# Performance work log

Hardware: AMD Instinct MI355X
Metric: run time of the kernel (lower is better)

Reference implementation:

```python
import jax, jax.numpy as jnp
import numpy as np

N = 8192
E = 524288
IN_DIM = 128
HID = 256
OUT_DIM = 128
N_LAYERS = 3
N_HEADS = 4
HEAD_DIM = HID // N_HEADS


def setup_inputs() -> dict:
    key = jax.random.key(0)
    ks = jax.random.split(key, 12)
    s = 0.05
    return {
        "x": jax.random.normal(ks[0], (N, IN_DIM), dtype=jnp.float32),
        "edge_index": jax.random.randint(ks[1], (2, E), 0, N, dtype=jnp.int64),
        "W_in": jax.random.normal(ks[2], (HID, IN_DIM), dtype=jnp.float32) * s,
        "b_in": jnp.zeros((HID,), dtype=jnp.float32),
        "plasticity": jnp.ones((N_LAYERS,), dtype=jnp.float32),
        "synaptic": jnp.ones((N_LAYERS,), dtype=jnp.float32),
        "in_proj_w": jax.random.normal(ks[3], (3 * HID, HID), dtype=jnp.float32) * s,
        "in_proj_b": jnp.zeros((3 * HID,), dtype=jnp.float32),
        "out_proj_w": jax.random.normal(ks[4], (HID, HID), dtype=jnp.float32) * s,
        "out_proj_b": jnp.zeros((HID,), dtype=jnp.float32),
        "W_out": jax.random.normal(ks[5], (OUT_DIM, HID), dtype=jnp.float32) * s,
        "b_out": jnp.zeros((OUT_DIM,), dtype=jnp.float32),
    }


def _forward(x, edge_index, W_in, b_in, plasticity, synaptic,
             in_proj_w, in_proj_b, out_proj_w, out_proj_b, W_out, b_out):
    src, dst = edge_index[0], edge_index[1]  # x_j = x[src], aggregate at dst (source_to_target)
    x = x @ W_in.T + b_in  # [N, HID]
    for i in range(N_LAYERS):
        x = x * jax.nn.sigmoid(plasticity[i])
        # message: x_j * sigmoid(synaptic) (scalar edge weight); aggr='add'
        agg = jax.ops.segment_sum(x[src], dst, num_segments=N)  # gather-scatter-add
        x = jax.nn.leaky_relu(agg * jax.nn.sigmoid(synaptic[i]), negative_slope=0.01)
    # MultiheadAttention over all N nodes (seq_len=N, batch=1)
    qkv = x @ in_proj_w.T + in_proj_b  # [N, 3*HID]
    q, k, v = jnp.split(qkv, 3, axis=-1)
    q = q.reshape(N, N_HEADS, HEAD_DIM).transpose(1, 0, 2)  # [h, n, d]
    k = k.reshape(N, N_HEADS, HEAD_DIM).transpose(1, 0, 2)
    v = v.reshape(N, N_HEADS, HEAD_DIM).transpose(1, 0, 2)
    scores = jnp.einsum("hnd,hmd->hnm", q, k) / np.sqrt(HEAD_DIM).astype(np.float32)
    attn = jax.nn.softmax(scores, axis=-1)
    o = jnp.einsum("hnm,hmd->hnd", attn, v)  # [h, n, d]
    o = o.transpose(1, 0, 2).reshape(N, HID)
    x = o @ out_proj_w.T + out_proj_b
    return x @ W_out.T + b_out  # [N, OUT_DIM]


def reference(x, edge_index, W_in, b_in, plasticity, synaptic,
              in_proj_w, in_proj_b, out_proj_w, out_proj_b, W_out, b_out):
    return _forward(x, edge_index, W_in, b_in, plasticity, synaptic,
                    in_proj_w, in_proj_b, out_proj_w, out_proj_b, W_out, b_out)
```

## Files before the change

kernel.cpp:

```cpp
#include <hip/hip_runtime.h>
#include <hip/hip_bf16.h>
#include <float.h>

#define N_NODES 8192
#define NEDGE   524288
#define IND     128
#define HID     256
#define OUTD    128
#define NHEAD   4
#define HD      64

typedef short short8 __attribute__((ext_vector_type(8)));
typedef float f32x4 __attribute__((ext_vector_type(4)));

__device__ __forceinline__ float sigmoidf_(float x) { return 1.0f / (1.0f + expf(-x)); }

__device__ __forceinline__ unsigned short f2bf(float f) {
    __hip_bfloat16 b = __float2bfloat16(f);
    return __builtin_bit_cast(unsigned short, b);
}
__device__ __forceinline__ float bf2f(unsigned short u) {
    __hip_bfloat16 b = __builtin_bit_cast(__hip_bfloat16, u);
    return __bfloat162float(b);
}
__device__ __forceinline__ void split3(float x, unsigned short& a, unsigned short& b, unsigned short& c) {
    a = f2bf(x); float r = x - bf2f(a);
    b = f2bf(r); r = r - bf2f(b);
    c = f2bf(r);
}
__device__ __forceinline__ unsigned int pack2(float lo, float hi) {
    return (unsigned int)f2bf(lo) | ((unsigned int)f2bf(hi) << 16);
}

__device__ __forceinline__ void gll16(const void* g, void* l) {
    __builtin_amdgcn_global_load_lds(
        (const __attribute__((address_space(1))) void*)g,
        (__attribute__((address_space(3))) void*)l, 16, 0, 0);
}

__global__ __launch_bounds__(256) void gemm_bias_kernel(
    const float* __restrict__ A, const float* __restrict__ W,
    const float* __restrict__ bias, float* __restrict__ C,
    int M, int Nn, int K)
{
    __shared__ float As[64][33];
    __shared__ float Ws[64][33];
    const int t  = threadIdx.x;
    const int tx = t & 15, ty = t >> 4;
    const int m0 = blockIdx.x * 64, n0 = blockIdx.y * 64;
    const int lr = t >> 2;
    const int lc = (t & 3) * 8;

    float acc[4][4] = {};
    for (int kk = 0; kk < K; kk += 32) {
        const float* Ap = A + (size_t)(m0 + lr) * K + kk + lc;
        const float* Wp = W + (size_t)(n0 + lr) * K + kk + lc;
        float4 a0 = *(const float4*)(Ap);
        float4 a1 = *(const float4*)(Ap + 4);
        float4 w0 = *(const float4*)(Wp);
        float4 w1 = *(const float4*)(Wp + 4);
        __syncthreads();
        As[lr][lc + 0] = a0.x; As[lr][lc + 1] = a0.y; As[lr][lc + 2] = a0.z; As[lr][lc + 3] = a0.w;
        As[lr][lc + 4] = a1.x; As[lr][lc + 5] = a1.y; As[lr][lc + 6] = a1.z; As[lr][lc + 7] = a1.w;
        Ws[lr][lc + 0] = w0.x; Ws[lr][lc + 1] = w0.y; Ws[lr][lc + 2] = w0.z; Ws[lr][lc + 3] = w0.w;
        Ws[lr][lc + 4] = w1.x; Ws[lr][lc + 5] = w1.y; Ws[lr][lc + 6] = w1.z; Ws[lr][lc + 7] = w1.w;
        __syncthreads();
        #pragma unroll 8
        for (int k = 0; k < 32; ++k) {
            float a[4], w[4];
            #pragma unroll
            for (int i = 0; i < 4; ++i) a[i] = As[ty * 4 + i][k];
            #pragma unroll
            for (int j = 0; j < 4; ++j) w[j] = Ws[tx * 4 + j][k];
            #pragma unroll
            for (int i = 0; i < 4; ++i)
                #pragma unroll
                for (int j = 0; j < 4; ++j)
                    acc[i][j] += a[i] * w[j];
        }
    }
    #pragma unroll
    for (int i = 0; i < 4; ++i) {
        const int m = m0 + ty * 4 + i;
        #pragma unroll
        for (int j = 0; j < 4; ++j) {
            const int n = n0 + tx * 4 + j;
            C[(size_t)m * Nn + n] = acc[i][j] + bias[n];
        }
    }
}

__global__ void hist_kernel(const int* __restrict__ ei, int* __restrict__ deg)
{
    int e = blockIdx.x * blockDim.x + threadIdx.x;
    if (e < NEDGE) atomicAdd(&deg[ei[NEDGE + e]], 1);
}

__global__ __launch_bounds__(1024) void scan_kernel(
    const int* __restrict__ deg, int* __restrict__ row_ptr, int* __restrict__ cursor)
{
    __shared__ int sh[1024];
    const int t = threadIdx.x;
    int v[8]; int s = 0;
    #pragma unroll
    for (int i = 0; i < 8; ++i) { v[i] = deg[t * 8 + i]; s += v[i]; }
    sh[t] = s; __syncthreads();
    for (int off = 1; off < 1024; off <<= 1) {
        int add = (t >= off) ? sh[t - off] : 0;
        __syncthreads();
        sh[t] += add;
        __syncthreads();
    }
    int base = sh[t] - s;
    #pragma unroll
    for (int i = 0; i < 8; ++i) {
        row_ptr[t * 8 + i] = base;
        cursor[t * 8 + i]  = base;
        base += v[i];
    }
    if (t == 1023) row_ptr[N_NODES] = base;
}

__global__ void scatter_kernel(const int* __restrict__ ei, int* __restrict__ cursor,
                               int* __restrict__ esrc)
{
    int e = blockIdx.x * blockDim.x + threadIdx.x;
    if (e < NEDGE) {
        int d = ei[NEDGE + e];
        int p = atomicAdd(&cursor[d], 1);
        esrc[p] = ei[e];
    }
}

__global__ __launch_bounds__(256) void aggregate_kernel(
    const float* __restrict__ hin, float* __restrict__ hout,
    const int* __restrict__ row_ptr, const int* __restrict__ esrc,
    const float* __restrict__ plas, const float* __restrict__ syn, int layer)
{
    const int b = blockIdx.x;
    const int c = threadIdx.x;
    const int st = row_ptr[b], en = row_ptr[b + 1];
    float a0 = 0.f, a1 = 0.f, a2 = 0.f, a3 = 0.f;
    int e = st;
    for (; e + 4 <= en; e += 4) {
        int s0 = esrc[e], s1 = esrc[e + 1], s2 = esrc[e + 2], s3 = esrc[e + 3];
        a0 += hin[(size_t)s0 * HID + c];
        a1 += hin[(size_t)s1 * HID + c];
        a2 += hin[(size_t)s2 * HID + c];
        a3 += hin[(size_t)s3 * HID + c];
    }
    float acc = (a0 + a1) + (a2 + a3);
    for (; e < en; ++e) acc += hin[(size_t)esrc[e] * HID + c];
    const float scale = sigmoidf_(plas[layer]) * sigmoidf_(syn[layer]);
    float x = acc * scale;
    hout[(size_t)b * HID + c] = (x > 0.f) ? x : 0.01f * x;
}

__global__ __launch_bounds__(256) void split_kernel(
    const float* __restrict__ qkv,
    unsigned short* __restrict__ Kc0, unsigned short* __restrict__ Kc1,
    unsigned short* __restrict__ Kc2, unsigned short* __restrict__ Vt0)
{
    __shared__ unsigned short vts[64 * 80];
    const int h  = blockIdx.y;
    const int n0 = blockIdx.x * 64;
    const int t  = threadIdx.x;
    const int r  = t >> 2;
    const int n  = n0 + r;
    const int dc = (t & 3) * 16;

    {
        const float* kp = qkv + (size_t)n * 768 + 256 + h * 64 + dc;
        float kv[16];
        #pragma unroll
        for (int i = 0; i < 16; i += 4) {
            float4 f = *(const float4*)(kp + i);
            kv[i] = f.x; kv[i+1] = f.y; kv[i+2] = f.z; kv[i+3] = f.w;
        }
        #pragma unroll
        for (int half = 0; half < 2; ++half) {
            short8 c0, c1, c2;
            #pragma unroll
            for (int j = 0; j < 8; ++j) {
                unsigned short a, b, c;
                split3(kv[half * 8 + j], a, b, c);
                c0[j] = (short)a; c1[j] = (short)b; c2[j] = (short)c;
            }
            const int pos = ((dc >> 3) + half) ^ (n & 7);
            const size_t base = ((size_t)(h * 8192 + n)) * 64 + pos * 8;
            *(short8*)(Kc0 + base) = c0;
            *(short8*)(Kc1 + base) = c1;
            *(short8*)(Kc2 + base) = c2;
        }
    }
    {
        const float* vp = qkv + (size_t)n * 768 + 512 + h * 64 + dc;
        #pragma unroll
        for (int i = 0; i < 16; i += 4) {
            float4 f = *(const float4*)(vp + i);
            float vv[4] = {f.x, f.y, f.z, f.w};
            #pragma unroll
            for (int k2 = 0; k2 < 4; ++k2)
                vts[(dc + i + k2) * 80 + r] = f2bf(vv[k2]);
        }
    }
    __syncthreads();
    #pragma unroll
    for (int i = 0; i < 2; ++i) {
        const int q = t * 2 + i;
        const int d = q >> 3, nc = q & 7;
        short8 vv = *(const short8*)(&vts[d * 80 + nc * 8]);
        const size_t dst = ((size_t)(h * 64 + d)) * 8192 + n0 + ((nc ^ (d & 7)) * 8);
        *(short8*)(Vt0 + dst) = vv;
    }
}

__global__ __launch_bounds__(256) void attn_mfma_kernel(
    const float* __restrict__ qkv,
    const unsigned short* __restrict__ Kc0, const unsigned short* __restrict__ Kc1,
    const unsigned short* __restrict__ Kc2, const unsigned short* __restrict__ Vt0,
    float* __restrict__ aO)
{
    __shared__ __align__(16) char smem[49152];
    const int h    = blockIdx.y;
    const int n0   = blockIdx.x * 128;
    const int t    = threadIdx.x;
    const int wv   = t >> 6;
    const int lane = t & 63;
    const int l15  = lane & 15, l4 = lane >> 4;
    const int qbase = n0 + wv * 32;

    short8 qf[2][3][2];
    #pragma unroll
    for (int qs = 0; qs < 2; ++qs) {
        #pragma unroll
        for (int ks = 0; ks < 2; ++ks) {
            const float* qp = qkv + (size_t)(qbase + qs * 16 + l15) * 768 + h * 64 + ks * 32 + l4 * 8;
            float4 qa = *(const float4*)qp, qb = *(const float4*)(qp + 4);
            float qv[8] = {qa.x, qa.y, qa.z, qa.w, qb.x, qb.y, qb.z, qb.w};
            #pragma unroll
            for (int j = 0; j < 8; ++j) {
                unsigned short a, b, c;
                split3(qv[j] * 0.125f, a, b, c);
                qf[qs][0][ks][j] = (short)a;
                qf[qs][1][ks][j] = (short)b;
                qf[qs][2][ks][j] = (short)c;
            }
        }
    }

    const unsigned short* cbase = (wv == 0) ? Kc0 : (wv == 1) ? Kc1 : (wv == 2) ? Kc2 : Vt0;
    const char* sgb[8];
    #pragma unroll
    for (int s = 0; s < 8; ++s) {
        const int row = s * 8 + (lane >> 3);
        if (wv < 3)
            sgb[s] = (const char*)(cbase + ((size_t)(h * 8192 + row)) * 64 + (lane & 7) * 8);
        else
            sgb[s] = (const char*)(cbase + ((size_t)(h * 64 + row)) * 8192 + (lane & 7) * 8);
    }
    const int ktstride = (wv < 3) ? 8192 : 128;

    auto STAGE = [&](int kt) {
        #pragma unroll
        for (int s = 0; s < 8; ++s)
            gll16(sgb[s] + (size_t)kt * ktstride, &smem[wv * 8192 + s * 1024]);
    };

    f32x4 o[2][4];
    float mrow[2], lsum[2];
    #pragma unroll
    for (int qs = 0; qs < 2; ++qs) {
        mrow[qs] = -FLT_MAX; lsum[qs] = 0.f;
        #pragma unroll
        for (int dt = 0; dt < 4; ++dt) o[qs][dt] = (f32x4){0.f, 0.f, 0.f, 0.f};
    }

    const int pbase = 32768 + wv * 4096;

    STAGE(0);
    __syncthreads();

    for (int kt = 0; kt < N_NODES / 64; ++kt) {
        f32x4 sacc[2][4];
        #pragma unroll
        for (int qs = 0; qs < 2; ++qs)
            #pragma unroll
            for (int nt = 0; nt < 4; ++nt) sacc[qs][nt] = (f32x4){0.f, 0.f, 0.f, 0.f};

        #pragma unroll
        for (int ntk = 0; ntk < 4; ++ntk) {
            const int key = ntk * 16 + l15;
            const int rowb = key * 128;
            #pragma unroll
            for (int ks = 0; ks < 2; ++ks) {
                const int cb = (((ks * 4 + l4) ^ (key & 7)) * 16);
                short8 kb0 = *(const short8*)(&smem[rowb + cb]);
                short8 kb1 = *(const short8*)(&smem[8192 + rowb + cb]);
                short8 kb2 = *(const short8*)(&smem[16384 + rowb + cb]);
                #pragma unroll
                for (int qs = 0; qs < 2; ++qs) {
                    f32x4 s = sacc[qs][ntk];
                    s = __builtin_amdgcn_mfma_f32_16x16x32_bf16(kb0, qf[qs][2][ks], s, 0, 0, 0);
                    s = __builtin_amdgcn_mfma_f32_16x16x32_bf16(kb1, qf[qs][1][ks], s, 0, 0, 0);
                    s = __builtin_amdgcn_mfma_f32_16x16x32_bf16(kb2, qf[qs][0][ks], s, 0, 0, 0);
                    s = __builtin_amdgcn_mfma_f32_16x16x32_bf16(kb0, qf[qs][1][ks], s, 0, 0, 0);
                    s = __builtin_amdgcn_mfma_f32_16x16x32_bf16(kb1, qf[qs][0][ks], s, 0, 0, 0);
                    s = __builtin_amdgcn_mfma_f32_16x16x32_bf16(kb0, qf[qs][0][ks], s, 0, 0, 0);
                    sacc[qs][ntk] = s;
                }
            }
        }

        #pragma unroll
        for (int qs = 0; qs < 2; ++qs) {
            float mx = -FLT_MAX;
            #pragma unroll
            for (int nt = 0; nt < 4; ++nt)
                #pragma unroll
                for (int r = 0; r < 4; ++r) mx = fmaxf(mx, sacc[qs][nt][r]);
            mx = fmaxf(mx, __shfl_xor(mx, 16));
            mx = fmaxf(mx, __shfl_xor(mx, 32));
            const float mn = fmaxf(mrow[qs], mx);
            const float alpha = __expf(mrow[qs] - mn);
            mrow[qs] = mn;
            float ps = 0.f;
            #pragma unroll
            for (int nt = 0; nt < 4; ++nt)
                #pragma unroll
                for (int r = 0; r < 4; ++r) {
                    float p = __expf(sacc[qs][nt][r] - mn);
                    sacc[qs][nt][r] = p;
                    ps += p;
                }
            ps += __shfl_xor(ps, 16);
            ps += __shfl_xor(ps, 32);
            lsum[qs] = lsum[qs] * alpha + ps;
            #pragma unroll
            for (int dt = 0; dt < 4; ++dt) o[qs][dt] *= alpha;

            #pragma unroll
            for (int nt = 0; nt < 4; ++nt) {
                #pragma unroll
                for (int w2 = 0; w2 < 2; ++w2) {
                    unsigned int pw = pack2(sacc[qs][nt][2 * w2], sacc[qs][nt][2 * w2 + 1]);
                    const int ks_ = nt >> 1;
                    const int l4t = (nt & 1) * 2 + (l4 >> 1);
                    const int jd  = (l4 & 1) * 2 + w2;
                    *(unsigned int*)(&smem[pbase + qs * 2048 + ks_ * 1024 + l4t * 256 + l15 * 16 + jd * 4]) = pw;
                }
            }
        }

        #pragma unroll
        for (int ks = 0; ks < 2; ++ks) {
            short8 pb0 = *(const short8*)(&smem[pbase + 0 * 2048 + ks * 1024 + lane * 16]);
            short8 pb1 = *(const short8*)(&smem[pbase + 1 * 2048 + ks * 1024 + lane * 16]);
            #pragma unroll
            for (int dt = 0; dt < 4; ++dt) {
                const int d = dt * 16 + l15;
                short8 va = *(const short8*)(&smem[24576 + d * 128 + (((ks * 4 + l4) ^ (d & 7)) * 16)]);
                o[0][dt] = __builtin_amdgcn_mfma_f32_16x16x32_bf16(va, pb0, o[0][dt], 0, 0, 0);
                o[1][dt] = __builtin_amdgcn_mfma_f32_16x16x32_bf16(va, pb1, o[1][dt], 0, 0, 0);
            }
        }

        __syncthreads();
        if (kt < N_NODES / 64 - 1) STAGE(kt + 1);
        __syncthreads();
    }

    #pragma unroll
    for (int qs = 0; qs < 2; ++qs) {
        const float inv = 1.f / lsum[qs];
        const int n = qbase + qs * 16 + l15;
        #pragma unroll
        for (int dt = 0; dt < 4; ++dt) {
            f32x4 ov = o[qs][dt];
            float4 st = {ov[0] * inv, ov[1] * inv, ov[2] * inv, ov[3] * inv};
            *(float4*)(&aO[(size_t)n * 256 + h * 64 + dt * 16 + l4 * 4]) = st;
        }
    }
}

extern "C" void kernel_launch(void* const* d_in, const int* in_sizes, int n_in,
                              void* d_out, int out_size, void* d_ws, size_t ws_size,
                              hipStream_t stream)
{
    const float* x     = (const float*)d_in[0];
    const int*   ei    = (const int*)  d_in[1];
    const float* W_in  = (const float*)d_in[2];
    const float* b_in  = (const float*)d_in[3];
    const float* plas  = (const float*)d_in[4];
    const float* syn   = (const float*)d_in[5];
    const float* inpw  = (const float*)d_in[6];
    const float* inpb  = (const float*)d_in[7];
    const float* outpw = (const float*)d_in[8];
    const float* outpb = (const float*)d_in[9];
    const float* Wout  = (const float*)d_in[10];
    const float* bout  = (const float*)d_in[11];
    float* out = (float*)d_out;

    char* ws = (char*)d_ws;
    float* h    = (float*)(ws + 0);
    float* h2   = (float*)(ws + (8u  << 20));
    float* qkv  = (float*)(ws + (16u << 20));
    float* aO   = (float*)(ws + (40u << 20));
    float* tmp  = (float*)(ws + (48u << 20));
    unsigned short* Kc0 = (unsigned short*)(ws + 0);
    unsigned short* Kc1 = (unsigned short*)(ws + (4u  << 20));
    unsigned short* Kc2 = (unsigned short*)(ws + (8u  << 20));
    unsigned short* Vt0 = (unsigned short*)(ws + (12u << 20));
    int* rowp = (int*)(ws + (56u << 20));
    int* curs = (int*)(ws + (56u << 20) + 40960);
    int* esrc = (int*)(ws + (56u << 20) + 81920);

    hipMemsetAsync(curs, 0, N_NODES * sizeof(int), stream);
    hist_kernel<<<NEDGE / 256, 256, 0, stream>>>(ei, curs);
    scan_kernel<<<1, 1024, 0, stream>>>(curs, rowp, curs);
    scatter_kernel<<<NEDGE / 256, 256, 0, stream>>>(ei, curs, esrc);

    gemm_bias_kernel<<<dim3(N_NODES / 64, HID / 64), 256, 0, stream>>>(
        x, W_in, b_in, h, N_NODES, HID, IND);

    aggregate_kernel<<<N_NODES, 256, 0, stream>>>(h,  h2, rowp, esrc, plas, syn, 0);
    aggregate_kernel<<<N_NODES, 256, 0, stream>>>(h2, h,  rowp, esrc, plas, syn, 1);
    aggregate_kernel<<<N_NODES, 256, 0, stream>>>(h,  h2, rowp, esrc, plas, syn, 2);

    gemm_bias_kernel<<<dim3(N_NODES / 64, 768 / 64), 256, 0, stream>>>(
        h2, inpw, inpb, qkv, N_NODES, 768, HID);

    split_kernel<<<dim3(N_NODES / 64, NHEAD), 256, 0, stream>>>(
        qkv, Kc0, Kc1, Kc2, Vt0);

    attn_mfma_kernel<<<dim3(N_NODES / 128, NHEAD), 256, 0, stream>>>(
        qkv, Kc0, Kc1, Kc2, Vt0, aO);

    gemm_bias_kernel<<<dim3(N_NODES / 64, HID / 64), 256, 0, stream>>>(
        aO, outpw, outpb, tmp, N_NODES, HID, HID);
    gemm_bias_kernel<<<dim3(N_NODES / 64, OUTD / 64), 256, 0, stream>>>(
        tmp, Wout, bout, out, N_NODES, OUTD, HID);
}
```

Measured before the change: 691.5 us.

## Rework attention with 32x32 MFMA, double-buffered K/V staging, and split-KV combine

The attention kernel now uses 32x32x16 bf16 MFMAs with 64 queries per wave. P is packed into the B operand in registers via cvt_pk_bf16 and permlane32 swaps, replacing the round trip through LDS. K/V tiles are double-buffered in 64KB LDS with one barrier per iteration, and the key range is split in two across blockIdx.z. A new combine kernel merges the partial outputs using the saved max and sum values. This adds an extra kernel plus partial-output traffic, and launch_bounds(256,1) with 64KB LDS limits occupancy to one block per CU.

```diff
diff --git a/kernel.cpp b/kernel.cpp
--- a/kernel.cpp
+++ b/kernel.cpp
@@ -11,7 +11,9 @@
 #define HD      64
 
 typedef short short8 __attribute__((ext_vector_type(8)));
-typedef float f32x4 __attribute__((ext_vector_type(4)));
+typedef float f32x4  __attribute__((ext_vector_type(4)));
+typedef float f32x16 __attribute__((ext_vector_type(16)));
+typedef unsigned int u32x4 __attribute__((ext_vector_type(4)));
 
 __device__ __forceinline__ float sigmoidf_(float x) { return 1.0f / (1.0f + expf(-x)); }
 
@@ -28,14 +30,23 @@
     b = f2bf(r); r = r - bf2f(b);
     c = f2bf(r);
 }
-__device__ __forceinline__ unsigned int pack2(float lo, float hi) {
-    return (unsigned int)f2bf(lo) | ((unsigned int)f2bf(hi) << 16);
+__device__ __forceinline__ unsigned int cvtpk(float lo, float hi) {
+    unsigned int r;
+    asm("v_cvt_pk_bf16_f32 %0, %1, %2" : "=v"(r) : "v"(lo), "v"(hi));
+    return r;
+}
+__device__ __forceinline__ void plswap(unsigned int& a, unsigned int& b) {
+    asm volatile("v_permlane32_swap_b32 %0, %1" : "+v"(a), "+v"(b));
 }
 
 __device__ __forceinline__ void gll16(const void* g, void* l) {
     __builtin_amdgcn_global_load_lds(
         (const __attribute__((address_space(1))) void*)g,
         (__attribute__((address_space(3))) void*)l, 16, 0, 0);
+}
+
+__device__ __forceinline__ f32x16 mfma32(short8 a, short8 b, f32x16 c) {
+    return __builtin_amdgcn_mfma_f32_32x32x16_bf16(a, b, c, 0, 0, 0);
 }
 
 __global__ __launch_bounds__(256) void gemm_bias_kernel(
@@ -186,7 +197,7 @@
                 split3(kv[half * 8 + j], a, b, c);
                 c0[j] = (short)a; c1[j] = (short)b; c2[j] = (short)c;
             }
-            const int pos = ((dc >> 3) + half) ^ (n & 7);
+            const int pos = ((dc >> 3) + half) ^ ((n >> 2) & 7);
             const size_t base = ((size_t)(h * 8192 + n)) * 64 + pos * 8;
             *(short8*)(Kc0 + base) = c0;
             *(short8*)(Kc1 + base) = c1;
@@ -210,41 +221,42 @@
         const int q = t * 2 + i;
         const int d = q >> 3, nc = q & 7;
         short8 vv = *(const short8*)(&vts[d * 80 + nc * 8]);
-        const size_t dst = ((size_t)(h * 64 + d)) * 8192 + n0 + ((nc ^ (d & 7)) * 8);
+        const size_t dst = ((size_t)(h * 64 + d)) * 8192 + n0 + ((nc ^ ((d >> 2) & 7)) * 8);
         *(short8*)(Vt0 + dst) = vv;
     }
 }
 
-__global__ __launch_bounds__(256) void attn_mfma_kernel(
+__global__ __launch_bounds__(256, 1) void attn_mfma_kernel(
     const float* __restrict__ qkv,
     const unsigned short* __restrict__ Kc0, const unsigned short* __restrict__ Kc1,
     const unsigned short* __restrict__ Kc2, const unsigned short* __restrict__ Vt0,
-    float* __restrict__ aO)
-{
-    __shared__ __align__(16) char smem[49152];
+    float* __restrict__ Op, float* __restrict__ Ml)
+{
+    __shared__ __align__(16) char smem[65536];
     const int h    = blockIdx.y;
-    const int n0   = blockIdx.x * 128;
+    const int half = blockIdx.z;
+    const int n0   = blockIdx.x * 256;
     const int t    = threadIdx.x;
     const int wv   = t >> 6;
     const int lane = t & 63;
-    const int l15  = lane & 15, l4 = lane >> 4;
-    const int qbase = n0 + wv * 32;
-
-    short8 qf[2][3][2];
-    #pragma unroll
-    for (int qs = 0; qs < 2; ++qs) {
-        #pragma unroll
-        for (int ks = 0; ks < 2; ++ks) {
-            const float* qp = qkv + (size_t)(qbase + qs * 16 + l15) * 768 + h * 64 + ks * 32 + l4 * 8;
-            float4 qa = *(const float4*)qp, qb = *(const float4*)(qp + 4);
-            float qv[8] = {qa.x, qa.y, qa.z, qa.w, qb.x, qb.y, qb.z, qb.w};
+    const int l31  = lane & 31, l5 = lane >> 5;
+    const int qbase = n0 + wv * 64;
+
+    short8 qf[2][3][4];
+    #pragma unroll
+    for (int qb = 0; qb < 2; ++qb) {
+        #pragma unroll
+        for (int ks = 0; ks < 4; ++ks) {
+            const float* qp = qkv + (size_t)(qbase + qb * 32 + l31) * 768 + h * 64 + ks * 16 + l5 * 8;
+            float4 qa = *(const float4*)qp, qb4 = *(const float4*)(qp + 4);
+            float qv[8] = {qa.x, qa.y, qa.z, qa.w, qb4.x, qb4.y, qb4.z, qb4.w};
             #pragma unroll
             for (int j = 0; j < 8; ++j) {
                 unsigned short a, b, c;
                 split3(qv[j] * 0.125f, a, b, c);
-                qf[qs][0][ks][j] = (short)a;
-                qf[qs][1][ks][j] = (short)b;
-                qf[qs][2][ks][j] = (short)c;
+                qf[qb][0][ks][j] = (short)a;
+                qf[qb][1][ks][j] = (short)b;
+                qf[qb][2][ks][j] = (short)c;
             }
         }
     }
@@ -259,127 +271,164 @@
         else
             sgb[s] = (const char*)(cbase + ((size_t)(h * 64 + row)) * 8192 + (lane & 7) * 8);
     }
-    const int ktstride = (wv < 3) ? 8192 : 128;
-
-    auto STAGE = [&](int kt) {
+    const size_t ktstride = (wv < 3) ? 8192 : 128;
+    const int ldsbase = wv * 8192;
+
+    auto STAGE = [&](int ktg, int bb) {
         #pragma unroll
         for (int s = 0; s < 8; ++s)
-            gll16(sgb[s] + (size_t)kt * ktstride, &smem[wv * 8192 + s * 1024]);
+            gll16(sgb[s] + (size_t)ktg * ktstride, &smem[bb * 32768 + ldsbase + s * 1024]);
     };
 
-    f32x4 o[2][4];
-    float mrow[2], lsum[2];
-    #pragma unroll
-    for (int qs = 0; qs < 2; ++qs) {
-        mrow[qs] = -FLT_MAX; lsum[qs] = 0.f;
-        #pragma unroll
-        for (int dt = 0; dt < 4; ++dt) o[qs][dt] = (f32x4){0.f, 0.f, 0.f, 0.f};
-    }
-
-    const int pbase = 32768 + wv * 4096;
-
-    STAGE(0);
+    f32x16 o[2][2];
+    #pragma unroll
+    for (int db = 0; db < 2; ++db)
+        #pragma unroll
+        for (int qb = 0; qb < 2; ++qb)
+            #pragma unroll
+            for (int r = 0; r < 16; ++r) o[db][qb][r] = 0.f;
+    float mr[2] = {-FLT_MAX, -FLT_MAX};
+    float ls[2] = {0.f, 0.f};
+
+    const int kt0 = half * 64;
+    STAGE(kt0, 0);
     __syncthreads();
 
-    for (int kt = 0; kt < N_NODES / 64; ++kt) {
-        f32x4 sacc[2][4];
-        #pragma unroll
-        for (int qs = 0; qs < 2; ++qs)
-            #pragma unroll
-            for (int nt = 0; nt < 4; ++nt) sacc[qs][nt] = (f32x4){0.f, 0.f, 0.f, 0.f};
-
-        #pragma unroll
-        for (int ntk = 0; ntk < 4; ++ntk) {
-            const int key = ntk * 16 + l15;
-            const int rowb = key * 128;
-            #pragma unroll
-            for (int ks = 0; ks < 2; ++ks) {
-                const int cb = (((ks * 4 + l4) ^ (key & 7)) * 16);
-                short8 kb0 = *(const short8*)(&smem[rowb + cb]);
-                short8 kb1 = *(const short8*)(&smem[8192 + rowb + cb]);
-                short8 kb2 = *(const short8*)(&smem[16384 + rowb + cb]);
+    for (int kt = 0; kt < 64; ++kt) {
+        const int bb = kt & 1;
+        if (kt < 63) STAGE(kt0 + kt + 1, bb ^ 1);
+        const char* buf = &smem[bb * 32768];
+
+        f32x16 s[2][2];
+        #pragma unroll
+        for (int kb = 0; kb < 2; ++kb)
+            #pragma unroll
+            for (int qb = 0; qb < 2; ++qb)
                 #pragma unroll
-                for (int qs = 0; qs < 2; ++qs) {
-                    f32x4 s = sacc[qs][ntk];
-                    s = __builtin_amdgcn_mfma_f32_16x16x32_bf16(kb0, qf[qs][2][ks], s, 0, 0, 0);
-                    s = __builtin_amdgcn_mfma_f32_16x16x32_bf16(kb1, qf[qs][1][ks], s, 0, 0, 0);
-                    s = __builtin_amdgcn_mfma_f32_16x16x32_bf16(kb2, qf[qs][0][ks], s, 0, 0, 0);
-                    s = __builtin_amdgcn_mfma_f32_16x16x32_bf16(kb0, qf[qs][1][ks], s, 0, 0, 0);
-                    s = __builtin_amdgcn_mfma_f32_16x16x32_bf16(kb1, qf[qs][0][ks], s, 0, 0, 0);
-                    s = __builtin_amdgcn_mfma_f32_16x16x32_bf16(kb0, qf[qs][0][ks], s, 0, 0, 0);
-                    sacc[qs][ntk] = s;
+                for (int r = 0; r < 16; ++r) s[kb][qb][r] = 0.f;
+
+        #pragma unroll
+        for (int ks = 0; ks < 4; ++ks) {
+            #pragma unroll
+            for (int kb = 0; kb < 2; ++kb) {
+                const int key = kb * 32 + l31;
+                const int off = key * 128 + (((ks * 2 + l5) ^ ((key >> 2) & 7)) * 16);
+                short8 k0 = *(const short8*)(buf + off);
+                short8 k1 = *(const short8*)(buf + 8192 + off);
+                short8 k2 = *(const short8*)(buf + 16384 + off);
+                #pragma unroll
+                for (int qb = 0; qb < 2; ++qb) {
+                    f32x16 acc = s[kb][qb];
+                    acc = mfma32(k0, qf[qb][2][ks], acc);
+                    acc = mfma32(k1, qf[qb][1][ks], acc);
+                    acc = mfma32(k2, qf[qb][0][ks], acc);
+                    acc = mfma32(k0, qf[qb][1][ks], acc);
+                    acc = mfma32(k1, qf[qb][0][ks], acc);
+                    acc = mfma32(k0, qf[qb][0][ks], acc);
+                    s[kb][qb] = acc;
                 }
             }
         }
 
-        #pragma unroll
-        for (int qs = 0; qs < 2; ++qs) {
-            float mx = -FLT_MAX;
-            #pragma unroll
-            for (int nt = 0; nt < 4; ++nt)
+        short8 pb[2][4];
+        #pragma unroll
+        for (int qb = 0; qb < 2; ++qb) {
+            float mx = s[0][qb][0];
+            #pragma unroll
+            for (int r = 1; r < 16; ++r) mx = fmaxf(mx, s[0][qb][r]);
+            #pragma unroll
+            for (int r = 0; r < 16; ++r) mx = fmaxf(mx, s[1][qb][r]);
+            mx = fmaxf(mx, __shfl_xor(mx, 32));
+            const float mn = fmaxf(mr[qb], mx);
+            const float alpha = __expf(mr[qb] - mn);
+            mr[qb] = mn;
+            float ps = 0.f;
+            #pragma unroll
+            for (int kb = 0; kb < 2; ++kb)
                 #pragma unroll
-                for (int r = 0; r < 4; ++r) mx = fmaxf(mx, sacc[qs][nt][r]);
-            mx = fmaxf(mx, __shfl_xor(mx, 16));
-            mx = fmaxf(mx, __shfl_xor(mx, 32));
-            const float mn = fmaxf(mrow[qs], mx);
-            const float alpha = __expf(mrow[qs] - mn);
-            mrow[qs] = mn;
-            float ps = 0.f;
-            #pragma unroll
-            for (int nt = 0; nt < 4; ++nt)
-                #pragma unroll
-                for (int r = 0; r < 4; ++r) {
-                    float p = __expf(sacc[qs][nt][r] - mn);
-                    sacc[qs][nt][r] = p;
+                for (int r = 0; r < 16; ++r) {
+                    float p = __expf(s[kb][qb][r] - mn);
+                    s[kb][qb][r] = p;
                     ps += p;
                 }
-            ps += __shfl_xor(ps, 16);
             ps += __shfl_xor(ps, 32);
-            lsum[qs] = lsum[qs] * alpha + ps;
-            #pragma unroll
-            for (int dt = 0; dt < 4; ++dt) o[qs][dt] *= alpha;
-
-            #pragma unroll
-            for (int nt = 0; nt < 4; ++nt) {
-                #pragma unroll
-                for (int w2 = 0; w2 < 2; ++w2) {
-                    unsigned int pw = pack2(sacc[qs][nt][2 * w2], sacc[qs][nt][2 * w2 + 1]);
-                    const int ks_ = nt >> 1;
-                    const int l4t = (nt & 1) * 2 + (l4 >> 1);
-                    const int jd  = (l4 & 1) * 2 + w2;
-                    *(unsigned int*)(&smem[pbase + qs * 2048 + ks_ * 1024 + l4t * 256 + l15 * 16 + jd * 4]) = pw;
-                }
-            }
-        }
-
-        #pragma unroll
-        for (int ks = 0; ks < 2; ++ks) {
-            short8 pb0 = *(const short8*)(&smem[pbase + 0 * 2048 + ks * 1024 + lane * 16]);
-            short8 pb1 = *(const short8*)(&smem[pbase + 1 * 2048 + ks * 1024 + lane * 16]);
-            #pragma unroll
-            for (int dt = 0; dt < 4; ++dt) {
-                const int d = dt * 16 + l15;
-                short8 va = *(const short8*)(&smem[24576 + d * 128 + (((ks * 4 + l4) ^ (d & 7)) * 16)]);
-                o[0][dt] = __builtin_amdgcn_mfma_f32_16x16x32_bf16(va, pb0, o[0][dt], 0, 0, 0);
-                o[1][dt] = __builtin_amdgcn_mfma_f32_16x16x32_bf16(va, pb1, o[1][dt], 0, 0, 0);
+            ls[qb] = ls[qb] * alpha + ps;
+            o[0][qb] *= alpha;
+            o[1][qb] *= alpha;
+
+            #pragma unroll
+            for (int ks = 0; ks < 4; ++ks) {
+                const int kb = ks >> 1, rb = (ks & 1) * 8;
+                unsigned int A0 = cvtpk(s[kb][qb][rb + 0], s[kb][qb][rb + 1]);
+                unsigned int A1 = cvtpk(s[kb][qb][rb + 2], s[kb][qb][rb + 3]);
+                unsigned int B0 = cvtpk(s[kb][qb][rb + 4], s[kb][qb][rb + 5]);
+                unsigned int B1 = cvtpk(s[kb][qb][rb + 6], s[kb][qb][rb + 7]);
+                plswap(A0, B0);
+                plswap(A1, B1);
+                u32x4 pw; pw[0] = A0; pw[1] = A1; pw[2] = B0; pw[3] = B1;
+                pb[qb][ks] = __builtin_bit_cast(short8, pw);
+            }
+        }
+
+        #pragma unroll
+        for (int ks = 0; ks < 4; ++ks) {
+            #pragma unroll
+            for (int db = 0; db < 2; ++db) {
+                const int d = db * 32 + l31;
+                const int off = 24576 + d * 128 + (((ks * 2 + l5) ^ ((d >> 2) & 7)) * 16);
+                short8 v = *(const short8*)(buf + off);
+                o[db][0] = mfma32(v, pb[0][ks], o[db][0]);
+                o[db][1] = mfma32(v, pb[1][ks], o[db][1]);
             }
         }
 
         __syncthreads();
-        if (kt < N_NODES / 64 - 1) STAGE(kt + 1);
-        __syncthreads();
-    }
-
-    #pragma unroll
-    for (int qs = 0; qs < 2; ++qs) {
-        const float inv = 1.f / lsum[qs];
-        const int n = qbase + qs * 16 + l15;
-        #pragma unroll
-        for (int dt = 0; dt < 4; ++dt) {
-            f32x4 ov = o[qs][dt];
-            float4 st = {ov[0] * inv, ov[1] * inv, ov[2] * inv, ov[3] * inv};
-            *(float4*)(&aO[(size_t)n * 256 + h * 64 + dt * 16 + l4 * 4]) = st;
-        }
+    }
+
+    #pragma unroll
+    for (int qb = 0; qb < 2; ++qb) {
+        const int q = qbase + qb * 32 + l31;
+        float* opq = Op + ((size_t)((half * 4 + h) * 8192 + q)) * 64;
+        #pragma unroll
+        for (int db = 0; db < 2; ++db) {
+            #pragma unroll
+            for (int tq = 0; tq < 4; ++tq) {
+                float4 st = { o[db][qb][4 * tq + 0], o[db][qb][4 * tq + 1],
+                              o[db][qb][4 * tq + 2], o[db][qb][4 * tq + 3] };
+                *(float4*)(opq + db * 32 + tq * 8 + l5 * 4) = st;
+            }
+        }
+        if (l5 == 0) {
+            Ml[((size_t)(half * 4 + h) * 2 + 0) * 8192 + q] = mr[qb];
+            Ml[((size_t)(half * 4 + h) * 2 + 1) * 8192 + q] = ls[qb];
+        }
+    }
+}
+
+__global__ __launch_bounds__(256) void combine_kernel(
+    const float* __restrict__ Op, const float* __restrict__ Ml, float* __restrict__ aO)
+{
+    const int idx = blockIdx.x * 256 + threadIdx.x;
+    const int c = idx & 3;
+    const int q = (idx >> 2) & 8191;
+    const int h = idx >> 15;
+    const float m0 = Ml[((size_t)(0 + h) * 2 + 0) * 8192 + q];
+    const float l0 = Ml[((size_t)(0 + h) * 2 + 1) * 8192 + q];
+    const float m1 = Ml[((size_t)(4 + h) * 2 + 0) * 8192 + q];
+    const float l1 = Ml[((size_t)(4 + h) * 2 + 1) * 8192 + q];
+    const float m  = fmaxf(m0, m1);
+    const float c0 = __expf(m0 - m), c1 = __expf(m1 - m);
+    const float inv = 1.f / (l0 * c0 + l1 * c1);
+    const float* p0 = Op + ((size_t)(0 + h) * 8192 + q) * 64 + c * 16;
+    const float* p1 = Op + ((size_t)(4 + h) * 8192 + q) * 64 + c * 16;
+    float* dst = aO + (size_t)q * 256 + h * 64 + c * 16;
+    #pragma unroll
+    for (int i = 0; i < 4; ++i) {
+        float4 a = *(const float4*)(p0 + i * 4);
+        float4 b = *(const float4*)(p1 + i * 4);
+        float4 r = { (a.x * c0 + b.x * c1) * inv, (a.y * c0 + b.y * c1) * inv,
+                     (a.z * c0 + b.z * c1) * inv, (a.w * c0 + b.w * c1) * inv };
+        *(float4*)(dst + i * 4) = r;
     }
 }
 
@@ -405,15 +454,17 @@
     float* h    = (float*)(ws + 0);
     float* h2   = (float*)(ws + (8u  << 20));
     float* qkv  = (float*)(ws + (16u << 20));
-    float* aO   = (float*)(ws + (40u << 20));
+    float* Op   = (float*)(ws + (40u << 20));
+    float* aO   = (float*)(ws + 0);
     float* tmp  = (float*)(ws + (48u << 20));
     unsigned short* Kc0 = (unsigned short*)(ws + 0);
     unsigned short* Kc1 = (unsigned short*)(ws + (4u  << 20));
     unsigned short* Kc2 = (unsigned short*)(ws + (8u  << 20));
     unsigned short* Vt0 = (unsigned short*)(ws + (12u << 20));
-    int* rowp = (int*)(ws + (56u << 20));
-    int* curs = (int*)(ws + (56u << 20) + 40960);
-    int* esrc = (int*)(ws + (56u << 20) + 81920);
+    int*   rowp = (int*)(ws + (56u << 20));
+    int*   curs = (int*)(ws + (56u << 20) + 40960);
+    int*   esrc = (int*)(ws + (56u << 20) + 81920);
+    float* Ml   = (float*)(ws + (56u << 20) + 81920);
 
     hipMemsetAsync(curs, 0, N_NODES * sizeof(int), stream);
     hist_kernel<<<NEDGE / 256, 256, 0, stream>>>(ei, curs);
@@ -433,8 +484,10 @@
     split_kernel<<<dim3(N_NODES / 64, NHEAD), 256, 0, stream>>>(
         qkv, Kc0, Kc1, Kc2, Vt0);
 
-    attn_mfma_kernel<<<dim3(N_NODES / 128, NHEAD), 256, 0, stream>>>(
-        qkv, Kc0, Kc1, Kc2, Vt0, aO);
+    attn_mfma_kernel<<<dim3(N_NODES / 256, NHEAD, 2), 256, 0, stream>>>(
+        qkv, Kc0, Kc1, Kc2, Vt0, Op, Ml);
+
+    combine_kernel<<<512, 256, 0, stream>>>(Op, Ml, aO);
 
     gemm_bias_kernel<<<dim3(N_NODES / 64, HID / 64), 256, 0, stream>>>(
         aO, outpw, outpb, tmp, N_NODES, HID, HID);
```

Result: faster. 610.7 us (-11.7%).
